# Kernel tuning notes

Hardware: AMD Instinct MI355X
Metric: run time of the kernel (lower is better)

The kernel has to match this reference:

```python
import math
import jax, jax.numpy as jnp
import numpy as np

N_HEADS = 8


def setup_inputs() -> dict:
    key = jax.random.key(0)
    k1, k2 = jax.random.split(key)
    bs, H, ch, T = 2, N_HEADS, 64, 2048
    qkv = jax.random.normal(k1, (bs, 3 * H * ch, T), dtype=jnp.float32)
    Weight_Mat = jax.random.uniform(k2, (bs * H, T, T), dtype=jnp.float32)
    return {"qkv": qkv, "Weight_Mat": Weight_Mat}


def reference(qkv, Weight_Mat):
    bs, width, length = qkv.shape
    assert width % (3 * N_HEADS) == 0
    ch = width // (3 * N_HEADS)
    q, k, v = jnp.split(qkv, 3, axis=1)
    scale = 1.0 / math.sqrt(math.sqrt(ch))
    q = (q * scale).reshape(bs * N_HEADS, ch, length)
    k = (k * scale).reshape(bs * N_HEADS, ch, length)
    # [bs*H, T, S] attention scores
    weight = jnp.einsum('bct,bcs->bts', q, k)
    weight = Weight_Mat * weight
    weight = jax.nn.softmax(weight.astype(jnp.float32), axis=-1).astype(weight.dtype)
    v = v.reshape(bs * N_HEADS, ch, length)
    a = jnp.einsum('bts,bcs->bct', weight, v)
    return a.reshape(bs, -1, length)
```

## Files before the change

### kernel.cpp

```cpp
#include <hip/hip_runtime.h>
#include <math.h>

#define TLEN 2048

typedef __attribute__((ext_vector_type(8))) short bf16x8;
typedef __attribute__((ext_vector_type(4))) float f32x4;

__device__ __forceinline__ unsigned fbits(float x){ union{float f; unsigned u;} a; a.f=x; return a.u; }
__device__ __forceinline__ float bitsf(unsigned u){ union{unsigned u; float f;} a; a.u=u; return a.f; }
__device__ __forceinline__ unsigned short f2b(float x){
  unsigned u = fbits(x);
  return (unsigned short)((u + 0x7fffu + ((u>>16)&1u)) >> 16);
}

__global__ __launch_bounds__(256, 2)
void wqkv_attn_mfma(const float* __restrict__ qkv,
                    const float* __restrict__ wm,
                    float* __restrict__ out) {
  const int bh = blockIdx.x & 15;
  const int t0 = (blockIdx.x >> 4) << 6;
  const int b  = bh >> 3;
  const int h  = bh & 7;
  const int tid  = threadIdx.x;
  const int w    = tid >> 6;
  const int lane = tid & 63;
  const int lt   = lane & 15;
  const int q4   = lane >> 4;

  __shared__ __align__(16) unsigned short Qhi[64][64], Qlo[64][64];
  __shared__ __align__(16) unsigned short Khi[64][72], Klo[64][72];
  __shared__ __align__(16) unsigned short Vhi[64][72], Vlo[64][72];
  __shared__ __align__(16) unsigned short Pl [64][72];

  const float* qb   = qkv + ((size_t)b*1536 + (size_t)h*64) * TLEN;
  const float* kb   = qb + (size_t)512  * TLEN;
  const float* vb   = qb + (size_t)1024 * TLEN;
  const float* wmat = wm + (size_t)bh * TLEN * TLEN;

  #pragma unroll
  for (int j = 0; j < 4; ++j) {
    int flat = tid + j*256;
    int c = flat >> 4, u = flat & 15;
    float4 v = *(const float4*)(qb + (size_t)c*TLEN + t0 + 4*u);
    float xs[4] = {v.x, v.y, v.z, v.w};
    #pragma unroll
    for (int i = 0; i < 4; ++i) {
      unsigned hb = fbits(xs[i]) & 0xffff0000u;
      Qhi[4*u+i][c] = (unsigned short)(hb >> 16);
      Qlo[4*u+i][c] = f2b(xs[i] - bitsf(hb));
    }
  }
  __syncthreads();

  bf16x8 qfh[2], qfl[2];
  #pragma unroll
  for (int kc = 0; kc < 2; ++kc) {
    qfh[kc] = *(const bf16x8*)&Qhi[16*w + lt][32*kc + 8*q4];
    qfl[kc] = *(const bf16x8*)&Qlo[16*w + lt][32*kc + 8*q4];
  }

  f32x4 accO[4];
  #pragma unroll
  for (int i = 0; i < 4; ++i) accO[i] = (f32x4){0.f,0.f,0.f,0.f};
  float m_run = -1e30f, l_run = 0.0f;

  for (int st = 0; st < 32; ++st) {
    const int s0 = st * 64;

    __syncthreads();

    float4 wv[4];
    #pragma unroll
    for (int fm = 0; fm < 4; ++fm)
      wv[fm] = *(const float4*)(wmat + (size_t)(t0 + 16*w + lt)*TLEN + s0 + 16*fm + 4*q4);

    #pragma unroll
    for (int j = 0; j < 4; ++j) {
      int flat = tid + j*256;
      int c = flat >> 4, u = flat & 15;
      float4 kv = *(const float4*)(kb + (size_t)c*TLEN + s0 + 4*u);
      int pc = c ^ (8*(u & 7));
      float ks[4] = {kv.x,kv.y,kv.z,kv.w};
      #pragma unroll
      for (int i = 0; i < 4; ++i) {
        unsigned hb = fbits(ks[i]) & 0xffff0000u;
        Khi[4*u+i][pc] = (unsigned short)(hb >> 16);
        Klo[4*u+i][pc] = f2b(ks[i] - bitsf(hb));
      }
      float4 vv = *(const float4*)(vb + (size_t)c*TLEN + s0 + 4*u);
      unsigned xh = (fbits(vv.x)>>16) | (fbits(vv.y) & 0xffff0000u);
      unsigned yh = (fbits(vv.z)>>16) | (fbits(vv.w) & 0xffff0000u);
      unsigned xl = (unsigned)f2b(vv.x - bitsf(fbits(vv.x)&0xffff0000u))
                  | ((unsigned)f2b(vv.y - bitsf(fbits(vv.y)&0xffff0000u)) << 16);
      unsigned yl = (unsigned)f2b(vv.z - bitsf(fbits(vv.z)&0xffff0000u))
                  | ((unsigned)f2b(vv.w - bitsf(fbits(vv.w)&0xffff0000u)) << 16);
      *(uint2*)&Vhi[c][4*u] = make_uint2(xh, yh);
      *(uint2*)&Vlo[c][4*u] = make_uint2(xl, yl);
    }
    __syncthreads();

    f32x4 acc[4];
    #pragma unroll
    for (int fm = 0; fm < 4; ++fm) {
      f32x4 a = (f32x4){0.f,0.f,0.f,0.f};
      const int srow = 16*fm + lt;
      const int f = (4*fm + (lt >> 2)) & 7;
      #pragma unroll
      for (int kc = 0; kc < 2; ++kc) {
        const int blk = (4*kc + q4) ^ f;
        bf16x8 kh = *(const bf16x8*)&Khi[srow][8*blk];
        bf16x8 kl = *(const bf16x8*)&Klo[srow][8*blk];
        a = __builtin_amdgcn_mfma_f32_16x16x32_bf16(kh, qfh[kc], a, 0,0,0);
        a = __builtin_amdgcn_mfma_f32_16x16x32_bf16(kh, qfl[kc], a, 0,0,0);
        a = __builtin_amdgcn_mfma_f32_16x16x32_bf16(kl, qfh[kc], a, 0,0,0);
      }
      acc[fm] = a;
    }

    float sv[4][4];
    float mx = -1e30f;
    #pragma unroll
    for (int fm = 0; fm < 4; ++fm) {
      float wvf[4] = {wv[fm].x, wv[fm].y, wv[fm].z, wv[fm].w};
      #pragma unroll
      for (int r = 0; r < 4; ++r) {
        float x = acc[fm][r] * 0.125f * wvf[r];
        sv[fm][r] = x;
        mx = fmaxf(mx, x);
      }
    }
    mx = fmaxf(mx, __shfl_xor(mx, 16));
    mx = fmaxf(mx, __shfl_xor(mx, 32));
    const float mn   = fmaxf(m_run, mx);
    const float corr = __expf(m_run - mn);
    m_run = mn;
    float sum = 0.f;
    unsigned short pb[4][4];
    #pragma unroll
    for (int fm = 0; fm < 4; ++fm)
      #pragma unroll
      for (int r = 0; r < 4; ++r) {
        float p = __expf(sv[fm][r] - mn);
        sum += p;
        pb[fm][r] = f2b(p);
      }
    sum += __shfl_xor(sum, 16);
    sum += __shfl_xor(sum, 32);
    l_run = l_run * corr + sum;
    #pragma unroll
    for (int fm = 0; fm < 4; ++fm)
      #pragma unroll
      for (int r = 0; r < 4; ++r)
        accO[fm][r] *= corr;

    #pragma unroll
    for (int fm = 0; fm < 4; ++fm) {
      unsigned p01 = (unsigned)pb[fm][0] | ((unsigned)pb[fm][1] << 16);
      unsigned p23 = (unsigned)pb[fm][2] | ((unsigned)pb[fm][3] << 16);
      *(uint2*)&Pl[16*w + lt][16*fm + 4*q4] = make_uint2(p01, p23);
    }

    #pragma unroll
    for (int kc = 0; kc < 2; ++kc) {
      bf16x8 pf = *(const bf16x8*)&Pl[16*w + lt][32*kc + 8*q4];
      #pragma unroll
      for (int fm = 0; fm < 4; ++fm) {
        bf16x8 vh = *(const bf16x8*)&Vhi[16*fm + lt][32*kc + 8*q4];
        bf16x8 vl = *(const bf16x8*)&Vlo[16*fm + lt][32*kc + 8*q4];
        accO[fm] = __builtin_amdgcn_mfma_f32_16x16x32_bf16(vh, pf, accO[fm], 0,0,0);
        accO[fm] = __builtin_amdgcn_mfma_f32_16x16x32_bf16(vl, pf, accO[fm], 0,0,0);
      }
    }
  }

  const float inv = 1.0f / l_run;
  #pragma unroll
  for (int fm = 0; fm < 4; ++fm)
    #pragma unroll
    for (int r = 0; r < 4; ++r) {
      int c = 16*fm + 4*q4 + r;
      out[((size_t)b*512 + (size_t)h*64 + c)*TLEN + t0 + 16*w + lt] = accO[fm][r] * inv;
    }
}

extern "C" void kernel_launch(void* const* d_in, const int* in_sizes, int n_in,
                              void* d_out, int out_size, void* d_ws, size_t ws_size,
                              hipStream_t stream) {
  const float* qkv = (const float*)d_in[0];
  const float* wm  = (const float*)d_in[1];
  float* out = (float*)d_out;
  dim3 grid(512);
  dim3 block(256);
  hipLaunchKernelGGL(wqkv_attn_mfma, grid, block, 0, stream, qkv, wm, out);
}
```

Baseline: 397.1 us.

## Prefetch next K/V/W tile into registers and raise MFMA wave priority

Restructures the main loop into a two-stage register double buffer: the K, V and Weight_Mat loads for tile st+1 are issued right after the LDS staging barrier of tile st, so global latency overlaps the MFMA and softmax work of the current tile. The loop is unrolled by two with swapped buffer sets, and the barrier moves to the end of each tile body. It also wraps the MFMA sections with s_setprio to favour waves doing matrix math. The extra 48 float registers per thread for the prefetch buffers may raise register pressure against the launch bound of 2 blocks per CU.

Result: no change. 401.1 us (+1.0%).

```diff
diff --git a/kernel.cpp b/kernel.cpp
--- a/kernel.cpp
+++ b/kernel.cpp
@@ -64,30 +64,39 @@
   for (int i = 0; i < 4; ++i) accO[i] = (f32x4){0.f,0.f,0.f,0.f};
   float m_run = -1e30f, l_run = 0.0f;
 
-  for (int st = 0; st < 32; ++st) {
-    const int s0 = st * 64;
-
-    __syncthreads();
-
-    float4 wv[4];
-    #pragma unroll
-    for (int fm = 0; fm < 4; ++fm)
-      wv[fm] = *(const float4*)(wmat + (size_t)(t0 + 16*w + lt)*TLEN + s0 + 16*fm + 4*q4);
-
+  const int stg_c = tid >> 4;
+  (void)stg_c;
+
+  auto load_kv = [&](int s0n, float4 (&kN)[4], float4 (&vN)[4]) {
     #pragma unroll
     for (int j = 0; j < 4; ++j) {
       int flat = tid + j*256;
       int c = flat >> 4, u = flat & 15;
-      float4 kv = *(const float4*)(kb + (size_t)c*TLEN + s0 + 4*u);
+      kN[j] = *(const float4*)(kb + (size_t)c*TLEN + s0n + 4*u);
+      vN[j] = *(const float4*)(vb + (size_t)c*TLEN + s0n + 4*u);
+    }
+  };
+  auto load_w = [&](int s0n, float4 (&wN)[4]) {
+    #pragma unroll
+    for (int fm = 0; fm < 4; ++fm)
+      wN[fm] = *(const float4*)(wmat + (size_t)(t0 + 16*w + lt)*TLEN + s0n + 16*fm + 4*q4);
+  };
+
+  auto tile_body = [&](int st, float4 (&kC)[4], float4 (&vC)[4], float4 (&wC)[4],
+                               float4 (&kN)[4], float4 (&vN)[4], float4 (&wN)[4]) {
+    #pragma unroll
+    for (int j = 0; j < 4; ++j) {
+      int flat = tid + j*256;
+      int c = flat >> 4, u = flat & 15;
       int pc = c ^ (8*(u & 7));
-      float ks[4] = {kv.x,kv.y,kv.z,kv.w};
+      float ks[4] = {kC[j].x, kC[j].y, kC[j].z, kC[j].w};
       #pragma unroll
       for (int i = 0; i < 4; ++i) {
         unsigned hb = fbits(ks[i]) & 0xffff0000u;
         Khi[4*u+i][pc] = (unsigned short)(hb >> 16);
         Klo[4*u+i][pc] = f2b(ks[i] - bitsf(hb));
       }
-      float4 vv = *(const float4*)(vb + (size_t)c*TLEN + s0 + 4*u);
+      float4 vv = vC[j];
       unsigned xh = (fbits(vv.x)>>16) | (fbits(vv.y) & 0xffff0000u);
       unsigned yh = (fbits(vv.z)>>16) | (fbits(vv.w) & 0xffff0000u);
       unsigned xl = (unsigned)f2b(vv.x - bitsf(fbits(vv.x)&0xffff0000u))
@@ -99,7 +108,13 @@
     }
     __syncthreads();
 
+    if (st + 1 < 32) {
+      load_kv((st+1)*64, kN, vN);
+      load_w ((st+1)*64, wN);
+    }
+
     f32x4 acc[4];
+    __builtin_amdgcn_s_setprio(1);
     #pragma unroll
     for (int fm = 0; fm < 4; ++fm) {
       f32x4 a = (f32x4){0.f,0.f,0.f,0.f};
@@ -116,12 +131,13 @@
       }
       acc[fm] = a;
     }
+    __builtin_amdgcn_s_setprio(0);
 
     float sv[4][4];
     float mx = -1e30f;
     #pragma unroll
     for (int fm = 0; fm < 4; ++fm) {
-      float wvf[4] = {wv[fm].x, wv[fm].y, wv[fm].z, wv[fm].w};
+      float wvf[4] = {wC[fm].x, wC[fm].y, wC[fm].z, wC[fm].w};
       #pragma unroll
       for (int r = 0; r < 4; ++r) {
         float x = acc[fm][r] * 0.125f * wvf[r];
@@ -160,6 +176,7 @@
       *(uint2*)&Pl[16*w + lt][16*fm + 4*q4] = make_uint2(p01, p23);
     }
 
+    __builtin_amdgcn_s_setprio(1);
     #pragma unroll
     for (int kc = 0; kc < 2; ++kc) {
       bf16x8 pf = *(const bf16x8*)&Pl[16*w + lt][32*kc + 8*q4];
@@ -171,6 +188,17 @@
         accO[fm] = __builtin_amdgcn_mfma_f32_16x16x32_bf16(vl, pf, accO[fm], 0,0,0);
       }
     }
+    __builtin_amdgcn_s_setprio(0);
+
+    __syncthreads();
+  };
+
+  float4 kA[4], vA[4], wA[4], kB[4], vB[4], wB[4];
+  load_kv(0, kA, vA);
+  load_w (0, wA);
+  for (int st = 0; st < 32; st += 2) {
+    tile_body(st,     kA, vA, wA, kB, vB, wB);
+    tile_body(st + 1, kB, vB, wB, kA, vA, wA);
   }
 
   const float inv = 1.0f / l_run;
```
